# Kernel optimization log

Hardware: AMD Instinct MI355X
Metric: run time of the kernel (lower is better)

The kernel has to match this reference:

```python
import jax, jax.numpy as jnp
import numpy as np

N_LOCS = 100000
N_TIMES = 169
N_USERS = 50000
LOC_DIM = 64
TIME_DIM = 32
USER_DIM = 32
N_HIDDEN = 64
EMB_DIM = LOC_DIM + TIME_DIM + USER_DIM  # 128
OUT_DIM = 2 * N_HIDDEN  # 128
N = 1_000_000


def setup_inputs() -> dict:
    key = jax.random.key(0)
    ks = jax.random.split(key, 8)
    x = jax.random.randint(ks[0], (N, 1), 0, N_LOCS, dtype=jnp.int32)
    t = jax.random.randint(ks[1], (N, 1), 0, N_TIMES, dtype=jnp.int32)
    u = jax.random.randint(ks[2], (N,), 0, N_USERS, dtype=jnp.int32)
    loc_emb = jax.random.normal(ks[3], (N_LOCS, LOC_DIM), jnp.float32) * 0.02
    time_emb = jax.random.normal(ks[4], (N_TIMES, TIME_DIM), jnp.float32) * 0.02
    user_emb = jax.random.normal(ks[5], (N_USERS + 1, USER_DIM), jnp.float32) * 0.02
    user_emb = user_emb.at[0].set(0.0)  # padding_idx=0
    W = jax.random.normal(ks[6], (OUT_DIM, EMB_DIM), jnp.float32) * (1.0 / np.sqrt(EMB_DIM))
    b = jax.random.normal(ks[7], (OUT_DIM,), jnp.float32) * 0.01
    return {"loc_emb": loc_emb, "time_emb": time_emb, "user_emb": user_emb,
            "W": W, "b": b, "x": x, "t": t, "u": u}


def _argunique(x0, t0):
    # hash = t*(x.max()+1) + x, sort, dedupe (padded to N for static shapes)
    n = x0.shape[0]
    h = t0 * (x0.max() + 1) + x0
    idcs = jnp.argsort(h)            # stable sort
    sh = h[idcs]
    mask = jnp.concatenate([jnp.ones((1,), bool), sh[1:] != sh[:-1]])
    group = jnp.cumsum(mask) - 1     # group id per sorted position
    inv = jnp.zeros((n,), jnp.int32).at[idcs].set(group.astype(jnp.int32))
    first_pos = jax.ops.segment_min(jnp.arange(n), group, num_segments=n)
    unique_idcs = idcs[jnp.clip(first_pos, 0, n - 1)]  # rows >= n_unique invalid
    counts = jax.ops.segment_sum(jnp.ones((n,), jnp.float32), group, num_segments=n)
    n_unique = mask.sum()
    return unique_idcs, inv, counts, n_unique


def reference(loc_emb, time_emb, user_emb, W, b, x, t, u):
    n = x.shape[0]
    unique_idcs, inv, counts, n_unique = _argunique(x[:, 0], t[:, 0])
    x_u = x[unique_idcs, 0]
    t_u = t[unique_idcs, 0]
    xt_embed = jnp.concatenate([loc_emb[x_u], time_emb[t_u]], axis=-1)  # [N, 96]
    ui_embed = user_emb[u]                                             # [N, 32]
    u_sum = jax.ops.segment_sum(ui_embed, inv, num_segments=n)         # scatter-add
    u_mean = u_sum / jnp.maximum(counts, 1.0)[:, None]                 # group mean
    xtu = jnp.concatenate([xt_embed, u_mean], axis=-1)                 # [N, 128]
    out = jnp.tanh(xtu @ W.T + b)
    valid = jnp.arange(n)[:, None] < n_unique  # rows past n_unique zeroed (padding)
    return jnp.where(valid, out, 0.0)
```

## Files before the change

kernel.cpp:

```cpp
#include <hip/hip_runtime.h>

#define WORDS    528384
#define NB_SCAN  258

#define IDX_SCALARS 0
#define IDX_MASK1   16
#define IDX_MASK2   (16 + WORDS)
#define IDX_COUNTS  (16 + 2*WORDS)
#define IDX_WBASE(nrows)  (16 + 2*WORDS + (nrows))
#define IDX_PART(nrows)   (IDX_WBASE(nrows) + WORDS)
#define IDX_PART2(nrows)  (IDX_PART(nrows) + 512)
#define IDX_HRANK(nrows)  (IDX_PART2(nrows) + 512)

typedef __attribute__((ext_vector_type(8))) short s8x;
typedef __attribute__((ext_vector_type(4))) float f4x;

__device__ __forceinline__ float tanh_fast(float z) {
    float e = __expf(2.0f * z);
    return 1.0f - 2.0f * __builtin_amdgcn_rcpf(e + 1.0f);
}

__device__ __forceinline__ unsigned bfr(float f) {
    unsigned u = __float_as_uint(f);
    return (u + 0x7FFFu + ((u >> 16) & 1u)) >> 16;
}

__device__ __forceinline__ void split8(const float* fv, s8x& hi, s8x& lo) {
    #pragma unroll
    for (int e = 0; e < 8; ++e) {
        unsigned hb = bfr(fv[e]);
        hi[e] = (short)hb;
        lo[e] = (short)bfr(fv[e] - __uint_as_float(hb << 16));
    }
}

__global__ void k_init(const int* __restrict__ x, unsigned* __restrict__ scalars, int n) {
    int g = blockIdx.x * blockDim.x + threadIdx.x;
    int row = g < n ? g : n - 1;
    unsigned v = (unsigned)x[row];
    #pragma unroll
    for (int off = 32; off > 0; off >>= 1) {
        unsigned o = (unsigned)__shfl_xor((int)v, off);
        v = v > o ? v : o;
    }
    if ((threadIdx.x & 63) == 0) atomicMax(scalars, v);
}

__global__ void k_bits(const int* __restrict__ x, const int* __restrict__ t,
                       const unsigned* __restrict__ scalars,
                       unsigned* __restrict__ mask1, unsigned* __restrict__ mask2, int n) {
    int g = blockIdx.x * blockDim.x + threadIdx.x;
    if (g >= n) return;
    unsigned d = scalars[0] + 1u;
    unsigned h = (unsigned)t[g] * d + (unsigned)x[g];
    unsigned w = h >> 5, bit = 1u << (h & 31);
    unsigned old = atomicOr(&mask1[w], bit);
    if (old & bit) atomicOr(&mask2[w], bit);
}

__global__ void k_scan1(const unsigned* __restrict__ mask1, unsigned* __restrict__ part) {
    const int t = threadIdx.x, b = blockIdx.x;
    const unsigned* wp = mask1 + (size_t)b * 2048 + t * 8;
    unsigned s = 0;
    #pragma unroll
    for (int i = 0; i < 8; ++i) s += __popc(wp[i]);
    #pragma unroll
    for (int off = 32; off > 0; off >>= 1) s += (unsigned)__shfl_xor((int)s, off);
    __shared__ unsigned red[4];
    if ((t & 63) == 0) red[t >> 6] = s;
    __syncthreads();
    if (t == 0) part[b] = red[0] + red[1] + red[2] + red[3];
}

__global__ void k_scan2(const unsigned* __restrict__ part, unsigned* __restrict__ part2,
                        unsigned* __restrict__ scalars) {
    const int t = threadIdx.x;
    __shared__ unsigned sm[512];
    unsigned v = (t < NB_SCAN) ? part[t] : 0u;
    sm[t] = v;
    __syncthreads();
    for (int off = 1; off < 512; off <<= 1) {
        unsigned add = (t >= off) ? sm[t - off] : 0u;
        __syncthreads();
        sm[t] += add;
        __syncthreads();
    }
    part2[t] = sm[t] - v;
    if (t == 511) scalars[1] = sm[511];
}

__global__ void k_scan3(const unsigned* __restrict__ mask1, const unsigned* __restrict__ part2,
                        unsigned* __restrict__ wbase) {
    const int t = threadIdx.x, b = blockIdx.x;
    const int lane = t & 63, wid = t >> 6;
    const size_t w0 = (size_t)b * 2048 + t * 8;
    unsigned pc[8], tsum = 0;
    #pragma unroll
    for (int i = 0; i < 8; ++i) { pc[i] = __popc(mask1[w0 + i]); tsum += pc[i]; }
    unsigned incl = tsum;
    #pragma unroll
    for (int off = 1; off < 64; off <<= 1) {
        unsigned vv = (unsigned)__shfl_up((int)incl, off);
        if (lane >= off) incl += vv;
    }
    __shared__ unsigned wt[4];
    if (lane == 63) wt[wid] = incl;
    __syncthreads();
    unsigned base = part2[b] + (incl - tsum);
    for (int i = 0; i < wid; ++i) base += wt[i];
    #pragma unroll
    for (int i = 0; i < 8; ++i) { wbase[w0 + i] = base; base += pc[i]; }
}

__global__ void k_zero_multi(const unsigned* __restrict__ mask1, const unsigned* __restrict__ mask2,
                             const unsigned* __restrict__ wbase, float* __restrict__ out) {
    int w = blockIdx.x * blockDim.x + threadIdx.x;
    if (w >= WORDS) return;
    unsigned m2 = mask2[w];
    if (!m2) return;
    unsigned m1 = mask1[w];
    unsigned base = wbase[w];
    float4 z = make_float4(0.f, 0.f, 0.f, 0.f);
    do {
        int b = __builtin_ctz(m2);
        m2 &= m2 - 1u;
        unsigned r = base + __popc(m1 & ((1u << b) - 1u));
        float4* dst = (float4*)(out + (size_t)r * 128 + 96);
        #pragma unroll
        for (int q = 0; q < 8; ++q) dst[q] = z;
    } while (m2);
}

__global__ void k_scatter(const int* __restrict__ x, const int* __restrict__ t,
                          const int* __restrict__ u, const float* __restrict__ user_emb,
                          const unsigned* __restrict__ scalars,
                          const unsigned* __restrict__ mask1, const unsigned* __restrict__ mask2,
                          const unsigned* __restrict__ wbase,
                          unsigned* __restrict__ counts, unsigned* __restrict__ hrank,
                          float* __restrict__ out, int n) {
    int j = blockIdx.x * blockDim.x + threadIdx.x;
    if (j >= n) return;
    unsigned d  = scalars[0] + 1u;
    unsigned xv = (unsigned)x[j], tv = (unsigned)t[j];
    unsigned h = tv * d + xv;
    unsigned w = h >> 5, bp = h & 31;
    unsigned r = wbase[w] + __popc(mask1[w] & ((1u << bp) - 1u));
    unsigned multi = (mask2[w] >> bp) & 1u;
    unsigned pack = xv | (tv << 17) | (multi << 31);
    hrank[r] = pack;
    if (!multi) {
        counts[r] = (unsigned)u[j];
    } else {
        atomicAdd(&counts[r], 1u);
        const float4* ue = (const float4*)(user_emb + (size_t)u[j] * 32);
        float* dst = out + (size_t)r * 128 + 96;
        #pragma unroll
        for (int q = 0; q < 8; ++q) {
            float4 v = ue[q];
            unsafeAtomicAdd(dst + q * 4 + 0, v.x);
            unsafeAtomicAdd(dst + q * 4 + 1, v.y);
            unsafeAtomicAdd(dst + q * 4 + 2, v.z);
            unsafeAtomicAdd(dst + q * 4 + 3, v.w);
        }
    }
}

__global__ __launch_bounds__(256, 2) void k_gemm(
    const float* __restrict__ loc_emb, const float* __restrict__ time_emb,
    const float* __restrict__ user_emb,
    const float* __restrict__ W, const float* __restrict__ bias,
    const unsigned* __restrict__ scalars, const unsigned* __restrict__ counts,
    const unsigned* __restrict__ hrank, float* __restrict__ out, int n) {
    const int tid  = threadIdx.x;
    const int wave = tid >> 6, lane = tid & 63;
    const int lr = lane & 15, lg = lane >> 4;
    const int wrow = wave & 1, wcol = wave >> 1;
    const int cbase = wcol * 64;
    const unsigned nu = scalars[1];

    s8x bhi[4][4], blo[4][4];
    {
        const float* wr = W + (size_t)(cbase + lr) * 128 + lg * 8;
        #pragma unroll
        for (int ct = 0; ct < 4; ++ct) {
            #pragma unroll
            for (int ks = 0; ks < 4; ++ks) {
                const float4* p = (const float4*)(wr + ct * 16 * 128 + ks * 32);
                float4 v0 = p[0], v1 = p[1];
                float fv[8] = {v0.x, v0.y, v0.z, v0.w, v1.x, v1.y, v1.z, v1.w};
                split8(fv, bhi[ct][ks], blo[ct][ks]);
            }
        }
    }
    float bv[4];
    #pragma unroll
    for (int ct = 0; ct < 4; ++ct) bv[ct] = bias[cbase + ct * 16 + lr];

    const int nstripes = (n + 63) >> 6;
    for (int stripe = blockIdx.x; stripe < nstripes; stripe += gridDim.x) {
        const int r0 = stripe * 64;
        if ((unsigned)r0 >= nu) {
            int rows = (n - r0 < 64) ? (n - r0) : 64;
            float4 z = make_float4(0.f, 0.f, 0.f, 0.f);
            float4* o4 = (float4*)(out + (size_t)r0 * 128);
            for (int i = tid; i < rows * 32; i += 256) o4[i] = z;
            continue;
        }
        const int rb = r0 + wrow * 32;

        unsigned xx[2], tt[2], cnt[2], mlt[2];
        bool val[2];
        #pragma unroll
        for (int rt = 0; rt < 2; ++rt) {
            unsigned r = (unsigned)(rb + rt * 16 + lr);
            val[rt] = r < nu;
            unsigned hv = val[rt] ? hrank[r] : 0u;
            xx[rt]  = hv & 0x1FFFFu;
            tt[rt]  = (hv >> 17) & 0xFFu;
            mlt[rt] = hv >> 31;
            cnt[rt] = val[rt] ? counts[r] : 0u;
        }

        f4x acc[2][4];
        {
            f4x z = {0.f, 0.f, 0.f, 0.f};
            #pragma unroll
            for (int rt = 0; rt < 2; ++rt)
                #pragma unroll
                for (int ct = 0; ct < 4; ++ct) acc[rt][ct] = z;
        }

        #pragma unroll
        for (int ks = 0; ks < 4; ++ks) {
            s8x ahi[2], alo[2];
            #pragma unroll
            for (int rt = 0; rt < 2; ++rt) {
                if (val[rt]) {
                    const float4* p;
                    float sc = 1.0f;
                    if (ks == 0)      p = (const float4*)(loc_emb  + (size_t)xx[rt] * 64 + lg * 8);
                    else if (ks == 1) p = (const float4*)(loc_emb  + (size_t)xx[rt] * 64 + 32 + lg * 8);
                    else if (ks == 2) p = (const float4*)(time_emb + (size_t)tt[rt] * 32 + lg * 8);
                    else {
                        if (mlt[rt]) {
                            p  = (const float4*)(out + (size_t)(rb + rt * 16 + lr) * 128 + 96 + lg * 8);
                            sc = __builtin_amdgcn_rcpf((float)cnt[rt]);
                        } else {
                            p  = (const float4*)(user_emb + (size_t)cnt[rt] * 32 + lg * 8);
                        }
                    }
                    float4 v0 = p[0], v1 = p[1];
                    float fv[8] = {v0.x * sc, v0.y * sc, v0.z * sc, v0.w * sc,
                                   v1.x * sc, v1.y * sc, v1.z * sc, v1.w * sc};
                    split8(fv, ahi[rt], alo[rt]);
                } else {
                    s8x z = {0, 0, 0, 0, 0, 0, 0, 0};
                    ahi[rt] = z; alo[rt] = z;
                }
            }
            #pragma unroll
            for (int ct = 0; ct < 4; ++ct) {
                #pragma unroll
                for (int rt = 0; rt < 2; ++rt) {
                    f4x c = acc[rt][ct];
                    c = __builtin_amdgcn_mfma_f32_16x16x32_bf16(ahi[rt], bhi[ct][ks], c, 0, 0, 0);
                    c = __builtin_amdgcn_mfma_f32_16x16x32_bf16(alo[rt], bhi[ct][ks], c, 0, 0, 0);
                    c = __builtin_amdgcn_mfma_f32_16x16x32_bf16(ahi[rt], blo[ct][ks], c, 0, 0, 0);
                    acc[rt][ct] = c;
                }
            }
        }

        __syncthreads();

        #pragma unroll
        for (int rt = 0; rt < 2; ++rt) {
            #pragma unroll
            for (int ct = 0; ct < 4; ++ct) {
                const int c = cbase + ct * 16 + lr;
                #pragma unroll
                for (int p = 0; p < 4; ++p) {
                    int rr = rb + rt * 16 + lg * 4 + p;
                    float o = 0.f;
                    if ((unsigned)rr < nu) o = tanh_fast(acc[rt][ct][p] + bv[ct]);
                    if (rr < n) out[(size_t)rr * 128 + c] = o;
                }
            }
        }
    }
}

extern "C" void kernel_launch(void* const* d_in, const int* in_sizes, int n_in,
                              void* d_out, int out_size, void* d_ws, size_t ws_size,
                              hipStream_t stream) {
    const float* loc_emb  = (const float*)d_in[0];
    const float* time_emb = (const float*)d_in[1];
    const float* user_emb = (const float*)d_in[2];
    const float* W        = (const float*)d_in[3];
    const float* bias     = (const float*)d_in[4];
    const int*   x        = (const int*)d_in[5];
    const int*   t        = (const int*)d_in[6];
    const int*   u        = (const int*)d_in[7];
    float* out = (float*)d_out;
    const int n = in_sizes[5];

    unsigned* ws32    = (unsigned*)d_ws;
    unsigned* scalars = ws32 + IDX_SCALARS;
    unsigned* mask1   = ws32 + IDX_MASK1;
    unsigned* mask2   = ws32 + IDX_MASK2;
    unsigned* counts  = ws32 + IDX_COUNTS;
    unsigned* wbase   = ws32 + IDX_WBASE(n);
    unsigned* part    = ws32 + IDX_PART(n);
    unsigned* part2   = ws32 + IDX_PART2(n);
    unsigned* hrank   = ws32 + IDX_HRANK(n);

    const size_t zero_bytes = (size_t)(16 + 2 * WORDS + n) * 4;
    hipMemsetAsync(d_ws, 0, zero_bytes, stream);

    int nb = (n + 255) / 256;
    k_init      <<<nb, 256, 0, stream>>>(x, scalars, n);
    k_bits      <<<nb, 256, 0, stream>>>(x, t, scalars, mask1, mask2, n);
    k_scan1     <<<NB_SCAN, 256, 0, stream>>>(mask1, part);
    k_scan2     <<<1, 512, 0, stream>>>(part, part2, scalars);
    k_scan3     <<<NB_SCAN, 256, 0, stream>>>(mask1, part2, wbase);
    k_zero_multi<<<(WORDS + 255) / 256, 256, 0, stream>>>(mask1, mask2, wbase, out);
    k_scatter   <<<nb, 256, 0, stream>>>(x, t, u, user_emb, scalars, mask1, mask2,
                                         wbase, counts, hrank, out, n);
    k_gemm      <<<3125, 256, 0, stream>>>(loc_emb, time_emb, user_emb, W, bias,
                                           scalars, counts, hrank, out, n);
}
```

Baseline: 1.115 ms.

## Drop split-bf16 compensation, swap MFMA operands for vectorized stores, raise occupancy

The GEMM stage stops emulating fp32 with hi/lo bf16 splits, so each product takes one bf16 MFMA instead of three and the operand conversion work shrinks. W and activation operands are swapped so each lane holds four consecutive output columns, letting results go out as float4 stores instead of scalar strided stores. Launch bounds rise to three blocks per CU, the gather pointers are precomputed once per stripe, and tanh uses a short polynomial for small arguments. The trade is lower numerical accuracy from single-bf16 inputs and a tanh approximation, which could exceed tolerance. The final bounds check on rr < n is also removed.

```diff
diff --git a/kernel.cpp b/kernel.cpp
--- a/kernel.cpp
+++ b/kernel.cpp
@@ -1,4 +1,5 @@
 #include <hip/hip_runtime.h>
+#include <hip/hip_bf16.h>
 
 #define WORDS    528384
 #define NB_SCAN  258
@@ -20,18 +21,26 @@
     return 1.0f - 2.0f * __builtin_amdgcn_rcpf(e + 1.0f);
 }
 
-__device__ __forceinline__ unsigned bfr(float f) {
-    unsigned u = __float_as_uint(f);
-    return (u + 0x7FFFu + ((u >> 16) & 1u)) >> 16;
-}
-
-__device__ __forceinline__ void split8(const float* fv, s8x& hi, s8x& lo) {
-    #pragma unroll
-    for (int e = 0; e < 8; ++e) {
-        unsigned hb = bfr(fv[e]);
-        hi[e] = (short)hb;
-        lo[e] = (short)bfr(fv[e] - __uint_as_float(hb << 16));
-    }
+__device__ __forceinline__ float tanh_poly(float z) {
+    float t = z * z;
+    float w = __builtin_fmaf(t, 0.13333333f, -0.33333333f);
+    float r = z * __builtin_fmaf(t, w, 1.0f);
+    if (__builtin_expect(__builtin_fabsf(z) > 0.25f, 0)) r = tanh_fast(z);
+    return r;
+}
+
+__device__ __forceinline__ short f2bf(float f) {
+    __hip_bfloat16 h = __float2bfloat16(f);
+    short s;
+    __builtin_memcpy(&s, &h, 2);
+    return s;
+}
+
+__device__ __forceinline__ s8x pack8(float4 a, float4 b) {
+    s8x r;
+    r[0] = f2bf(a.x); r[1] = f2bf(a.y); r[2] = f2bf(a.z); r[3] = f2bf(a.w);
+    r[4] = f2bf(b.x); r[5] = f2bf(b.y); r[6] = f2bf(b.z); r[7] = f2bf(b.w);
+    return r;
 }
 
 __global__ void k_init(const int* __restrict__ x, unsigned* __restrict__ scalars, int n) {
@@ -165,7 +174,7 @@
     }
 }
 
-__global__ __launch_bounds__(256, 2) void k_gemm(
+__global__ __launch_bounds__(256, 3) void k_gemm(
     const float* __restrict__ loc_emb, const float* __restrict__ time_emb,
     const float* __restrict__ user_emb,
     const float* __restrict__ W, const float* __restrict__ bias,
@@ -178,7 +187,7 @@
     const int cbase = wcol * 64;
     const unsigned nu = scalars[1];
 
-    s8x bhi[4][4], blo[4][4];
+    s8x wf[4][4];
     {
         const float* wr = W + (size_t)(cbase + lr) * 128 + lg * 8;
         #pragma unroll
@@ -186,15 +195,14 @@
             #pragma unroll
             for (int ks = 0; ks < 4; ++ks) {
                 const float4* p = (const float4*)(wr + ct * 16 * 128 + ks * 32);
-                float4 v0 = p[0], v1 = p[1];
-                float fv[8] = {v0.x, v0.y, v0.z, v0.w, v1.x, v1.y, v1.z, v1.w};
-                split8(fv, bhi[ct][ks], blo[ct][ks]);
+                wf[ct][ks] = pack8(p[0], p[1]);
             }
         }
     }
-    float bv[4];
-    #pragma unroll
-    for (int ct = 0; ct < 4; ++ct) bv[ct] = bias[cbase + ct * 16 + lr];
+    float4 bias4[4];
+    #pragma unroll
+    for (int ct = 0; ct < 4; ++ct)
+        bias4[ct] = ((const float4*)bias)[(cbase >> 2) + ct * 4 + lg];
 
     const int nstripes = (n + 63) >> 6;
     for (int stripe = blockIdx.x; stripe < nstripes; stripe += gridDim.x) {
@@ -208,17 +216,24 @@
         }
         const int rb = r0 + wrow * 32;
 
-        unsigned xx[2], tt[2], cnt[2], mlt[2];
-        bool val[2];
+        const float* pl[2]; const float* pt[2]; const float* pu[2];
+        float sc[2]; bool val[2];
         #pragma unroll
         for (int rt = 0; rt < 2; ++rt) {
-            unsigned r = (unsigned)(rb + rt * 16 + lr);
-            val[rt] = r < nu;
-            unsigned hv = val[rt] ? hrank[r] : 0u;
-            xx[rt]  = hv & 0x1FFFFu;
-            tt[rt]  = (hv >> 17) & 0xFFu;
-            mlt[rt] = hv >> 31;
-            cnt[rt] = val[rt] ? counts[r] : 0u;
+            int rr = rb + rt * 16 + lr;
+            val[rt] = (unsigned)rr < nu;
+            unsigned hv = val[rt] ? hrank[rr] : 0u;
+            unsigned cv = val[rt] ? counts[rr] : 0u;
+            unsigned xx = hv & 0x1FFFFu, tv = (hv >> 17) & 0xFFu;
+            pl[rt] = loc_emb  + (size_t)xx * 64 + lg * 8;
+            pt[rt] = time_emb + (size_t)tv * 32 + lg * 8;
+            if (hv >> 31) {
+                pu[rt] = out + (size_t)rr * 128 + 96 + lg * 8;
+                sc[rt] = __builtin_amdgcn_rcpf((float)cv);
+            } else {
+                pu[rt] = user_emb + (size_t)cv * 32 + lg * 8;
+                sc[rt] = 1.0f;
+            }
         }
 
         f4x acc[2][4];
@@ -232,59 +247,53 @@
 
         #pragma unroll
         for (int ks = 0; ks < 4; ++ks) {
-            s8x ahi[2], alo[2];
+            s8x av[2];
             #pragma unroll
             for (int rt = 0; rt < 2; ++rt) {
                 if (val[rt]) {
                     const float4* p;
-                    float sc = 1.0f;
-                    if (ks == 0)      p = (const float4*)(loc_emb  + (size_t)xx[rt] * 64 + lg * 8);
-                    else if (ks == 1) p = (const float4*)(loc_emb  + (size_t)xx[rt] * 64 + 32 + lg * 8);
-                    else if (ks == 2) p = (const float4*)(time_emb + (size_t)tt[rt] * 32 + lg * 8);
-                    else {
-                        if (mlt[rt]) {
-                            p  = (const float4*)(out + (size_t)(rb + rt * 16 + lr) * 128 + 96 + lg * 8);
-                            sc = __builtin_amdgcn_rcpf((float)cnt[rt]);
-                        } else {
-                            p  = (const float4*)(user_emb + (size_t)cnt[rt] * 32 + lg * 8);
-                        }
+                    if (ks == 0)      p = (const float4*)(pl[rt]);
+                    else if (ks == 1) p = (const float4*)(pl[rt] + 32);
+                    else if (ks == 2) p = (const float4*)(pt[rt]);
+                    else              p = (const float4*)(pu[rt]);
+                    float4 v0 = p[0], v1 = p[1];
+                    if (ks == 3) {
+                        float s = sc[rt];
+                        v0.x *= s; v0.y *= s; v0.z *= s; v0.w *= s;
+                        v1.x *= s; v1.y *= s; v1.z *= s; v1.w *= s;
                     }
-                    float4 v0 = p[0], v1 = p[1];
-                    float fv[8] = {v0.x * sc, v0.y * sc, v0.z * sc, v0.w * sc,
-                                   v1.x * sc, v1.y * sc, v1.z * sc, v1.w * sc};
-                    split8(fv, ahi[rt], alo[rt]);
+                    av[rt] = pack8(v0, v1);
                 } else {
                     s8x z = {0, 0, 0, 0, 0, 0, 0, 0};
-                    ahi[rt] = z; alo[rt] = z;
+                    av[rt] = z;
                 }
             }
             #pragma unroll
+            for (int ct = 0; ct < 4; ++ct)
+                #pragma unroll
+                for (int rt = 0; rt < 2; ++rt)
+                    acc[rt][ct] = __builtin_amdgcn_mfma_f32_16x16x32_bf16(
+                        wf[ct][ks], av[rt], acc[rt][ct], 0, 0, 0);
+        }
+
+        __syncthreads();
+
+        #pragma unroll
+        for (int rt = 0; rt < 2; ++rt) {
+            int rr = rb + rt * 16 + lr;
+            float* orow = out + (size_t)rr * 128 + cbase + lg * 4;
+            #pragma unroll
             for (int ct = 0; ct < 4; ++ct) {
-                #pragma unroll
-                for (int rt = 0; rt < 2; ++rt) {
-                    f4x c = acc[rt][ct];
-                    c = __builtin_amdgcn_mfma_f32_16x16x32_bf16(ahi[rt], bhi[ct][ks], c, 0, 0, 0);
-                    c = __builtin_amdgcn_mfma_f32_16x16x32_bf16(alo[rt], bhi[ct][ks], c, 0, 0, 0);
-                    c = __builtin_amdgcn_mfma_f32_16x16x32_bf16(ahi[rt], blo[ct][ks], c, 0, 0, 0);
-                    acc[rt][ct] = c;
+                float4 o;
+                if (val[rt]) {
+                    o.x = tanh_poly(acc[rt][ct][0] + bias4[ct].x);
+                    o.y = tanh_poly(acc[rt][ct][1] + bias4[ct].y);
+                    o.z = tanh_poly(acc[rt][ct][2] + bias4[ct].z);
+                    o.w = tanh_poly(acc[rt][ct][3] + bias4[ct].w);
+                } else {
+                    o = make_float4(0.f, 0.f, 0.f, 0.f);
                 }
-            }
-        }
-
-        __syncthreads();
-
-        #pragma unroll
-        for (int rt = 0; rt < 2; ++rt) {
-            #pragma unroll
-            for (int ct = 0; ct < 4; ++ct) {
-                const int c = cbase + ct * 16 + lr;
-                #pragma unroll
-                for (int p = 0; p < 4; ++p) {
-                    int rr = rb + rt * 16 + lg * 4 + p;
-                    float o = 0.f;
-                    if ((unsigned)rr < nu) o = tanh_fast(acc[rt][ct][p] + bv[ct]);
-                    if (rr < n) out[(size_t)rr * 128 + c] = o;
-                }
+                *(float4*)(orow + ct * 16) = o;
             }
         }
     }
```

Result: faster. 1.053 ms (-5.5%).
